# Performance work log

Measured on AMD Instinct MI355X. Metric: run time of the kernel, lower is better.

Reference implementation:

```python
import jax, jax.numpy as jnp
import numpy as np

N = 8192
F_IN = 256
F_OUT = 64
ALPHA = 0.2  # LeakyReLU negative slope
MASK_VAL = -9e15


def setup_inputs() -> dict:
    key = jax.random.key(0)
    k1, k2, k3, k4 = jax.random.split(key, 4)
    h = jax.random.normal(k1, (N, F_IN), dtype=jnp.float32)
    adj = jax.random.randint(k2, (N, N), 0, 2, dtype=jnp.int32)  # 0/1 dense adjacency
    # Parameters (original creates them inside forward with xavier init; here fixed inputs)
    W = jax.random.normal(k3, (F_IN, F_OUT), dtype=jnp.float32) * (1.414 * np.sqrt(2.0 / (F_IN + F_OUT)))
    a = jax.random.normal(k4, (2 * F_OUT, 1), dtype=jnp.float32) * (1.414 * np.sqrt(2.0 / (2 * F_OUT + 1)))
    return {"h": h, "adj": adj, "W": W, "a": a}


def reference(h, adj, W, a):
    # Wh: [N, F_OUT]
    Wh = h @ W
    # e_ij = LeakyReLU(a^T [Wh_i ; Wh_j]) computed via broadcast instead of the
    f_src = Wh @ a[:F_OUT, 0]   # [N] contribution of row node i
    f_dst = Wh @ a[F_OUT:, 0]   # [N] contribution of col node j
    e = jax.nn.leaky_relu(f_src[:, None] + f_dst[None, :], negative_slope=ALPHA)  # [N, N]
    # adj-masked row softmax
    scores = jnp.where(adj > 0, e, MASK_VAL)
    attention = jax.nn.softmax(scores, axis=1)
    # dropout omitted (deterministic eval reference)
    h_prime = attention @ Wh  # [N, F_OUT]
    return jax.nn.elu(h_prime)  # concat=True branch
```

## Files before the change

### kernel.cpp

```cpp
#include <hip/hip_runtime.h>
#include <hip/hip_bf16.h>

#define NN 8192
#define FIN 256
#define FOUT 64
#define L2E 1.4426950408889634f

typedef __attribute__((ext_vector_type(8))) short short8;
typedef __attribute__((ext_vector_type(4))) float f32x4;
typedef __attribute__((ext_vector_type(4))) int   iv4;

__device__ __forceinline__ unsigned short f2bf(float x){
  unsigned u = __float_as_uint(x);
  u += 0x7FFFu + ((u >> 16) & 1u);
  return (unsigned short)(u >> 16);
}

__global__ __launch_bounds__(256) void k_prep(const float* __restrict__ h,
    const float* __restrict__ W, const float* __restrict__ a,
    unsigned short* __restrict__ WhT, float* __restrict__ fs,
    float* __restrict__ fd, unsigned* __restrict__ gmax_u){
  __shared__ float Ws[128*64];
  __shared__ float hs[8][128];
  const int t = threadIdx.x, l = t & 63, wv = t >> 6;
  const int rb = blockIdx.x * 8;
  float acc0 = 0.f, acc1 = 0.f;
  for (int half = 0; half < 2; ++half){
    if (half) __syncthreads();
    for (int i = t; i < 2048; i += 256)
      ((float4*)Ws)[i] = ((const float4*)W)[half*2048 + i];
    {
      int rr = t >> 5, cc = t & 31;
      ((float4*)&hs[rr][0])[cc] =
          *(const float4*)(h + (size_t)(rb+rr)*FIN + half*128 + cc*4);
    }
    __syncthreads();
    #pragma unroll 8
    for (int k = 0; k < 128; ++k){
      float wval = Ws[k*64 + l];
      acc0 = fmaf(hs[wv*2+0][k], wval, acc0);
      acc1 = fmaf(hs[wv*2+1][k], wval, acc1);
    }
  }
  const int r0 = rb + wv*2, r1 = r0 + 1;
  float a1 = a[l], a2 = a[64 + l];
  float p0 = acc0*a1, q0 = acc0*a2, p1 = acc1*a1, q1 = acc1*a2;
  #pragma unroll
  for (int m = 1; m < 64; m <<= 1){
    p0 += __shfl_xor(p0, m); q0 += __shfl_xor(q0, m);
    p1 += __shfl_xor(p1, m); q1 += __shfl_xor(q1, m);
  }
  if (l == 0){
    fs[r0] = p0*L2E; fs[r1] = p1*L2E; fd[r0] = q0*L2E; fd[r1] = q1*L2E;
    atomicMax(gmax_u, __float_as_uint(q0*L2E + 64.0f));
    atomicMax(gmax_u, __float_as_uint(q1*L2E + 64.0f));
  }
  WhT[(size_t)l*NN + r0] = f2bf(acc0);
  WhT[(size_t)l*NN + r1] = f2bf(acc1);
}

struct Buf {
  iv4    a0, a1;
  float4 f0, f1;
  short8 w0, w1, w2, w3;
};

__device__ __forceinline__ void load_buf(Buf& b, const int* __restrict__ adj,
    unsigned a_off, const float* __restrict__ fd, unsigned f_off,
    const unsigned short* __restrict__ WhT, unsigned w_off, int s){
  const iv4* ap = (const iv4*)(adj + a_off + s*32);
  b.a0 = __builtin_nontemporal_load(ap);
  b.a1 = __builtin_nontemporal_load(ap + 1);
  b.f0 = *(const float4*)(fd + f_off + s*32);
  b.f1 = *(const float4*)(fd + f_off + s*32 + 4);
  b.w0 = *(const short8*)(WhT + w_off + s*32);
  b.w1 = *(const short8*)(WhT + w_off + s*32 + 16*NN);
  b.w2 = *(const short8*)(WhT + w_off + s*32 + 32*NN);
  b.w3 = *(const short8*)(WhT + w_off + s*32 + 48*NN);
}

__device__ __forceinline__ void step_buf(const Buf& b, float fsrL, float mL,
                                         f32x4* acc, float& s0, float& s1){
  const int   av[8] = {b.a0.x,b.a0.y,b.a0.z,b.a0.w, b.a1.x,b.a1.y,b.a1.z,b.a1.w};
  const float fv[8] = {b.f0.x,b.f0.y,b.f0.z,b.f0.w, b.f1.x,b.f1.y,b.f1.z,b.f1.w};
  float w[8];
  #pragma unroll
  for (int j = 0; j < 8; ++j){
    float x  = fsrL + fv[j];
    float tt = fmaxf(x, 0.2f*x);
    float e  = __builtin_amdgcn_exp2f(tt - mL);
    w[j] = (av[j] != 0) ? e : 0.0f;
  }
  s0 += (w[0]+w[2]) + (w[4]+w[6]);
  s1 += (w[1]+w[3]) + (w[5]+w[7]);
  short8 af;
  __hip_bfloat162* afp = (__hip_bfloat162*)&af;
  #pragma unroll
  for (int j = 0; j < 4; ++j)
    afp[j] = __float22bfloat162_rn(make_float2(w[2*j], w[2*j+1]));
  acc[0] = __builtin_amdgcn_mfma_f32_16x16x32_bf16(af, b.w0, acc[0], 0,0,0);
  acc[1] = __builtin_amdgcn_mfma_f32_16x16x32_bf16(af, b.w1, acc[1], 0,0,0);
  acc[2] = __builtin_amdgcn_mfma_f32_16x16x32_bf16(af, b.w2, acc[2], 0,0,0);
  acc[3] = __builtin_amdgcn_mfma_f32_16x16x32_bf16(af, b.w3, acc[3], 0,0,0);
}

__global__ __launch_bounds__(256, 4) void k_attn(const int* __restrict__ adj,
    const unsigned short* __restrict__ WhT, const float* __restrict__ fs,
    const float* __restrict__ fd, const unsigned* __restrict__ gmax_u,
    float* __restrict__ acc_out, float* __restrict__ s_out){
  const int l = threadIdx.x & 63;
  const int task = blockIdx.x*4 + (threadIdx.x >> 6);
  const int itile = task & 511, kchunk = task >> 9;
  const int ibase = itile*16, row = l & 15, quad = l >> 4;
  const float gmaxL = __uint_as_float(*gmax_u) - 64.0f;
  const float fsrL  = fs[ibase + row];
  const float xL    = fsrL + gmaxL;
  const float mL    = fmaxf(xL, 0.2f*xL);

  const unsigned koff  = (unsigned)kchunk*1024u + quad*8u;
  const unsigned a_off = (unsigned)(ibase+row)*NN + koff;
  const unsigned w_off = (unsigned)row*NN + koff;
  const unsigned f_off = koff;

  f32x4 acc[4];
  #pragma unroll
  for (int nb = 0; nb < 4; ++nb) acc[nb] = (f32x4){0.f,0.f,0.f,0.f};

  Buf b0, b1;
  load_buf(b0, adj, a_off, fd, f_off, WhT, w_off, 0);
  load_buf(b1, adj, a_off, fd, f_off, WhT, w_off, 1);

  float s0 = 0.f, s1 = 0.f;
  #pragma unroll 1
  for (int s = 0; s < 32; s += 2){
    step_buf(b0, fsrL, mL, acc, s0, s1);
    if (s+2 < 32) load_buf(b0, adj, a_off, fd, f_off, WhT, w_off, s+2);
    step_buf(b1, fsrL, mL, acc, s0, s1);
    if (s+3 < 32) load_buf(b1, adj, a_off, fd, f_off, WhT, w_off, s+3);
  }

  float sacc = s0 + s1;
  sacc += __shfl_xor(sacc, 16);
  sacc += __shfl_xor(sacc, 32);
  if (l < 16) s_out[kchunk*NN + ibase + l] = sacc;
  float* op = acc_out + ((size_t)kchunk*NN + ibase)*FOUT;
  #pragma unroll
  for (int nb = 0; nb < 4; ++nb)
    #pragma unroll
    for (int r = 0; r < 4; ++r)
      op[(quad*4 + r)*FOUT + nb*16 + row] = acc[nb][r];
}

__global__ __launch_bounds__(256) void k_out(const float* __restrict__ acc,
    const float* __restrict__ s, float* __restrict__ out){
  const int idx = blockIdx.x*256 + threadIdx.x;
  const int i = idx >> 6;
  float num = 0.f, den = 0.f;
  #pragma unroll
  for (int ks = 0; ks < 8; ++ks){
    num += acc[idx + (size_t)ks*(NN*FOUT)];
    den += s[i + ks*NN];
  }
  float x = num / den;
  out[idx] = (x > 0.f) ? x : (__expf(x) - 1.0f);
}

extern "C" void kernel_launch(void* const* d_in, const int* in_sizes, int n_in,
                              void* d_out, int out_size, void* d_ws, size_t ws_size,
                              hipStream_t stream){
  const float* h   = (const float*)d_in[0];
  const int*   adj = (const int*)d_in[1];
  const float* W   = (const float*)d_in[2];
  const float* a   = (const float*)d_in[3];
  char* ws = (char*)d_ws;
  unsigned short* WhT = (unsigned short*)ws;
  float*    fs     = (float*)(ws + (1u<<20));
  float*    fd     = (float*)(ws + (1u<<20) + 32768);
  unsigned* gmax_u = (unsigned*)(ws + (1u<<20) + 65536);
  float*    acc    = (float*)(ws + (2u<<20));
  float*    s_ws   = (float*)(ws + (20u<<20));

  (void)hipMemsetAsync(gmax_u, 0, 4, stream);
  k_prep<<<1024, 256, 0, stream>>>(h, W, a, WhT, fs, fd, gmax_u);
  k_attn<<<1024, 256, 0, stream>>>(adj, WhT, fs, fd, gmax_u, acc, s_ws);
  k_out<<<2048, 256, 0, stream>>>(acc, s_ws, (float*)d_out);
}
```

Measured before the change: 520.6 us.

## Share WhT and fd slabs across waves via double-buffered LDS in attention kernel

The attention kernel now gives each block four waves covering 64 consecutive rows of the same key chunk. Each 32-column slice of WhT and fd is loaded once per block into double-buffered LDS and then read by all four waves, where before every wave fetched it from global memory on its own. This cuts redundant global/L2 traffic for the B operand. The cost is two barriers per step and extra LDS stores and reads, in a kernel that is likely bound by streaming the adjacency matrix.

```diff
diff --git a/kernel.cpp b/kernel.cpp
--- a/kernel.cpp
+++ b/kernel.cpp
@@ -5,10 +5,17 @@
 #define FIN 256
 #define FOUT 64
 #define L2E 1.4426950408889634f
+#define PADK 40
 
 typedef __attribute__((ext_vector_type(8))) short short8;
 typedef __attribute__((ext_vector_type(4))) float f32x4;
 typedef __attribute__((ext_vector_type(4))) int   iv4;
+
+#define BAR() do { \
+  __asm__ __volatile__("s_waitcnt lgkmcnt(0)" ::: "memory"); \
+  __builtin_amdgcn_s_barrier(); \
+  __asm__ __volatile__("" ::: "memory"); \
+} while (0)
 
 __device__ __forceinline__ unsigned short f2bf(float x){
   unsigned u = __float_as_uint(x);
@@ -59,30 +66,20 @@
   WhT[(size_t)l*NN + r1] = f2bf(acc1);
 }
 
-struct Buf {
-  iv4    a0, a1;
-  float4 f0, f1;
-  short8 w0, w1, w2, w3;
-};
-
-__device__ __forceinline__ void load_buf(Buf& b, const int* __restrict__ adj,
-    unsigned a_off, const float* __restrict__ fd, unsigned f_off,
-    const unsigned short* __restrict__ WhT, unsigned w_off, int s){
-  const iv4* ap = (const iv4*)(adj + a_off + s*32);
-  b.a0 = __builtin_nontemporal_load(ap);
-  b.a1 = __builtin_nontemporal_load(ap + 1);
-  b.f0 = *(const float4*)(fd + f_off + s*32);
-  b.f1 = *(const float4*)(fd + f_off + s*32 + 4);
-  b.w0 = *(const short8*)(WhT + w_off + s*32);
-  b.w1 = *(const short8*)(WhT + w_off + s*32 + 16*NN);
-  b.w2 = *(const short8*)(WhT + w_off + s*32 + 32*NN);
-  b.w3 = *(const short8*)(WhT + w_off + s*32 + 48*NN);
-}
-
-__device__ __forceinline__ void step_buf(const Buf& b, float fsrL, float mL,
-                                         f32x4* acc, float& s0, float& s1){
-  const int   av[8] = {b.a0.x,b.a0.y,b.a0.z,b.a0.w, b.a1.x,b.a1.y,b.a1.z,b.a1.w};
-  const float fv[8] = {b.f0.x,b.f0.y,b.f0.z,b.f0.w, b.f1.x,b.f1.y,b.f1.z,b.f1.w};
+struct ABuf { iv4 a0, a1; };
+
+__device__ __forceinline__ void load_adj(ABuf& b, const int* __restrict__ adj,
+                                         unsigned a_off, int s){
+  const iv4* p = (const iv4*)(adj + a_off + s*32);
+  b.a0 = __builtin_nontemporal_load(p);
+  b.a1 = __builtin_nontemporal_load(p + 1);
+}
+
+__device__ __forceinline__ void attn_math(const ABuf& ab, f32x4 fv0, f32x4 fv1,
+    short8 w0, short8 w1, short8 w2, short8 w3,
+    float fsrL, float mL, f32x4* acc, float& s0, float& s1){
+  const int   av[8] = {ab.a0.x,ab.a0.y,ab.a0.z,ab.a0.w, ab.a1.x,ab.a1.y,ab.a1.z,ab.a1.w};
+  const float fv[8] = {fv0[0],fv0[1],fv0[2],fv0[3], fv1[0],fv1[1],fv1[2],fv1[3]};
   float w[8];
   #pragma unroll
   for (int j = 0; j < 8; ++j){
@@ -98,45 +95,87 @@
   #pragma unroll
   for (int j = 0; j < 4; ++j)
     afp[j] = __float22bfloat162_rn(make_float2(w[2*j], w[2*j+1]));
-  acc[0] = __builtin_amdgcn_mfma_f32_16x16x32_bf16(af, b.w0, acc[0], 0,0,0);
-  acc[1] = __builtin_amdgcn_mfma_f32_16x16x32_bf16(af, b.w1, acc[1], 0,0,0);
-  acc[2] = __builtin_amdgcn_mfma_f32_16x16x32_bf16(af, b.w2, acc[2], 0,0,0);
-  acc[3] = __builtin_amdgcn_mfma_f32_16x16x32_bf16(af, b.w3, acc[3], 0,0,0);
+  acc[0] = __builtin_amdgcn_mfma_f32_16x16x32_bf16(af, w0, acc[0], 0,0,0);
+  acc[1] = __builtin_amdgcn_mfma_f32_16x16x32_bf16(af, w1, acc[1], 0,0,0);
+  acc[2] = __builtin_amdgcn_mfma_f32_16x16x32_bf16(af, w2, acc[2], 0,0,0);
+  acc[3] = __builtin_amdgcn_mfma_f32_16x16x32_bf16(af, w3, acc[3], 0,0,0);
 }
 
 __global__ __launch_bounds__(256, 4) void k_attn(const int* __restrict__ adj,
     const unsigned short* __restrict__ WhT, const float* __restrict__ fs,
     const float* __restrict__ fd, const unsigned* __restrict__ gmax_u,
     float* __restrict__ acc_out, float* __restrict__ s_out){
-  const int l = threadIdx.x & 63;
-  const int task = blockIdx.x*4 + (threadIdx.x >> 6);
-  const int itile = task & 511, kchunk = task >> 9;
-  const int ibase = itile*16, row = l & 15, quad = l >> 4;
+  __shared__ unsigned short bslab[2][64*PADK];
+  __shared__ float fslab[2][32];
+  const int t = threadIdx.x, l = t & 63, wv = t >> 6;
+  const int g = blockIdx.x & 127;
+  const int kchunk = blockIdx.x >> 7;
+  const int row = l & 15, quad = l >> 4;
+  const int ibase = g*64 + wv*16;
+  const int irow  = ibase + row;
   const float gmaxL = __uint_as_float(*gmax_u) - 64.0f;
-  const float fsrL  = fs[ibase + row];
+  const float fsrL  = fs[irow];
   const float xL    = fsrL + gmaxL;
   const float mL    = fmaxf(xL, 0.2f*xL);
 
-  const unsigned koff  = (unsigned)kchunk*1024u + quad*8u;
-  const unsigned a_off = (unsigned)(ibase+row)*NN + koff;
-  const unsigned w_off = (unsigned)row*NN + koff;
-  const unsigned f_off = koff;
+  const unsigned jbase = (unsigned)kchunk*1024u;
+  const unsigned a_off = (unsigned)irow*8192u + jbase + (unsigned)quad*8u;
+  const unsigned sg_off = (unsigned)l*8192u + jbase + (unsigned)wv*8u;
+  const int      sl_off = l*PADK + wv*8;
 
   f32x4 acc[4];
   #pragma unroll
   for (int nb = 0; nb < 4; ++nb) acc[nb] = (f32x4){0.f,0.f,0.f,0.f};
 
-  Buf b0, b1;
-  load_buf(b0, adj, a_off, fd, f_off, WhT, w_off, 0);
-  load_buf(b1, adj, a_off, fd, f_off, WhT, w_off, 1);
+  {
+    short8 v = *(const short8*)(WhT + sg_off);
+    *(short8*)&bslab[0][sl_off] = v;
+    if (t < 32) fslab[0][t] = fd[jbase + t];
+  }
+  ABuf ab0, ab1;
+  load_adj(ab0, adj, a_off, 0);
+  load_adj(ab1, adj, a_off, 1);
 
   float s0 = 0.f, s1 = 0.f;
+  short8 nw; float nf = 0.f;
+
   #pragma unroll 1
   for (int s = 0; s < 32; s += 2){
-    step_buf(b0, fsrL, mL, acc, s0, s1);
-    if (s+2 < 32) load_buf(b0, adj, a_off, fd, f_off, WhT, w_off, s+2);
-    step_buf(b1, fsrL, mL, acc, s0, s1);
-    if (s+3 < 32) load_buf(b1, adj, a_off, fd, f_off, WhT, w_off, s+3);
+    BAR();
+    nw = *(const short8*)(WhT + sg_off + (s+1)*32);
+    if (t < 32) nf = fd[jbase + (s+1)*32 + t];
+    {
+      f32x4 fv0 = *(const f32x4*)&fslab[0][quad*8];
+      f32x4 fv1 = *(const f32x4*)&fslab[0][quad*8 + 4];
+      short8 w0 = *(const short8*)&bslab[0][( 0 + row)*PADK + quad*8];
+      short8 w1 = *(const short8*)&bslab[0][(16 + row)*PADK + quad*8];
+      short8 w2 = *(const short8*)&bslab[0][(32 + row)*PADK + quad*8];
+      short8 w3 = *(const short8*)&bslab[0][(48 + row)*PADK + quad*8];
+      attn_math(ab0, fv0, fv1, w0, w1, w2, w3, fsrL, mL, acc, s0, s1);
+    }
+    if (s + 2 < 32) load_adj(ab0, adj, a_off, s + 2);
+    *(short8*)&bslab[1][sl_off] = nw;
+    if (t < 32) fslab[1][t] = nf;
+
+    BAR();
+    if (s + 2 < 32){
+      nw = *(const short8*)(WhT + sg_off + (s+2)*32);
+      if (t < 32) nf = fd[jbase + (s+2)*32 + t];
+    }
+    {
+      f32x4 fv0 = *(const f32x4*)&fslab[1][quad*8];
+      f32x4 fv1 = *(const f32x4*)&fslab[1][quad*8 + 4];
+      short8 w0 = *(const short8*)&bslab[1][( 0 + row)*PADK + quad*8];
+      short8 w1 = *(const short8*)&bslab[1][(16 + row)*PADK + quad*8];
+      short8 w2 = *(const short8*)&bslab[1][(32 + row)*PADK + quad*8];
+      short8 w3 = *(const short8*)&bslab[1][(48 + row)*PADK + quad*8];
+      attn_math(ab1, fv0, fv1, w0, w1, w2, w3, fsrL, mL, acc, s0, s1);
+    }
+    if (s + 3 < 32) load_adj(ab1, adj, a_off, s + 3);
+    if (s + 2 < 32){
+      *(short8*)&bslab[0][sl_off] = nw;
+      if (t < 32) fslab[0][t] = nf;
+    }
   }
 
   float sacc = s0 + s1;
```

After: 497.1 us. 1.05x faster.
